# Optimization experiments

Hardware: AMD Instinct MI355X
Metric: run time of the kernel (lower is better)

Reference implementation:

```python
import jax, jax.numpy as jnp
import numpy as np

D, H, DFF, N = 256, 8, 2048, 100
B, T, M1, M2 = 64, 77, 400, 400
DH = D // H
EPS = 1e-5
NEG = -1e9


def _ln(x, w, b):
    m = jnp.mean(x, axis=-1, keepdims=True)
    v = jnp.mean((x - m) ** 2, axis=-1, keepdims=True)
    return (x - m) / jnp.sqrt(v + EPS) * w + b


def _mha(q_in, kv_in, in_w, in_b, out_w, out_b, kpm):
    # q_in: [Tq, D], kv_in: [Tk, D], in_w: [3D, D], kpm: [Tk] bool (True = pad)
    wq, wk, wv = in_w[:D], in_w[D:2 * D], in_w[2 * D:]
    bq, bk, bv = in_b[:D], in_b[D:2 * D], in_b[2 * D:]
    q = (q_in @ wq.T + bq).reshape(-1, H, DH)
    k = (kv_in @ wk.T + bk).reshape(-1, H, DH)
    v = (kv_in @ wv.T + bv).reshape(-1, H, DH)
    scores = jnp.einsum('qhd,khd->hqk', q, k) / np.sqrt(DH).astype(np.float32)
    scores = jnp.where(kpm[None, None, :], NEG, scores)
    attn = jax.nn.softmax(scores, axis=-1)
    out = jnp.einsum('hqk,khd->qhd', attn, v).reshape(-1, D)
    return out @ out_w.T + out_b


def _decoder(x, mem, tmask, mmask, saw, sab, saow, saob,
             caw, cab, caow, caob, l1w, l1b, l2w, l2b,
             n1w, n1b, n2w, n2b, n3w, n3b):
    # Post-norm TransformerDecoderLayer (eval mode, no dropout)
    x = _ln(x + _mha(x, x, saw, sab, saow, saob, tmask), n1w, n1b)
    x = _ln(x + _mha(x, mem, caw, cab, caow, caob, mmask), n2w, n2b)
    ff = jax.nn.relu(x @ l1w.T + l1b) @ l2w.T + l2b
    return _ln(x + ff, n3w, n3b)


def setup_inputs() -> dict:
    key = jax.random.key(0)
    ks = jax.random.split(key, 12)
    s = 0.02
    return {
        'text_embed': jax.random.normal(ks[0], (B, T, D), jnp.float32),
        'text_mask': jnp.zeros((B, T), bool),
        'im_embed1': jax.random.normal(ks[1], (B, M1, D), jnp.float32),
        'im_mask1': jnp.zeros((B, M1), bool),
        'im_embed2': jax.random.normal(ks[2], (B, M2, D), jnp.float32),
        'im_mask2': jnp.zeros((B, M2), bool),
        'sid': jax.random.randint(ks[3], (B,), 0, N),
        'sa_in_w': jax.random.normal(ks[4], (N, 3 * D, D), jnp.float32) * s,
        'sa_in_b': jnp.zeros((N, 3 * D), jnp.float32),
        'sa_out_w': jax.random.normal(ks[5], (N, D, D), jnp.float32) * s,
        'sa_out_b': jnp.zeros((N, D), jnp.float32),
        'ca_in_w': jax.random.normal(ks[6], (N, 3 * D, D), jnp.float32) * s,
        'ca_in_b': jnp.zeros((N, 3 * D), jnp.float32),
        'ca_out_w': jax.random.normal(ks[7], (N, D, D), jnp.float32) * s,
        'ca_out_b': jnp.zeros((N, D), jnp.float32),
        'lin1_w': jax.random.normal(ks[8], (N, DFF, D), jnp.float32) * s,
        'lin1_b': jnp.zeros((N, DFF), jnp.float32),
        'lin2_w': jax.random.normal(ks[9], (N, D, DFF), jnp.float32) * s,
        'lin2_b': jnp.zeros((N, D), jnp.float32),
        'ln1_w': jnp.ones((N, D), jnp.float32),
        'ln1_b': jnp.zeros((N, D), jnp.float32),
        'ln2_w': jnp.ones((N, D), jnp.float32),
        'ln2_b': jnp.zeros((N, D), jnp.float32),
        'ln3_w': jnp.ones((N, D), jnp.float32),
        'ln3_b': jnp.zeros((N, D), jnp.float32),
    }


def reference(text_embed, text_mask, im_embed1, im_mask1, im_embed2, im_mask2, sid,
              sa_in_w, sa_in_b, sa_out_w, sa_out_b,
              ca_in_w, ca_in_b, ca_out_w, ca_out_b,
              lin1_w, lin1_b, lin2_w, lin2_b,
              ln1_w, ln1_b, ln2_w, ln2_b, ln3_w, ln3_b):
    mem = jnp.concatenate([im_embed1, im_embed2], axis=1)    # [B, M1+M2, D]
    mmask = jnp.concatenate([im_mask1, im_mask2], axis=1)    # [B, M1+M2]
    params = tuple(p[sid] for p in (
        sa_in_w, sa_in_b, sa_out_w, sa_out_b,
        ca_in_w, ca_in_b, ca_out_w, ca_out_b,
        lin1_w, lin1_b, lin2_w, lin2_b,
        ln1_w, ln1_b, ln2_w, ln2_b, ln3_w, ln3_b))
    return jax.vmap(_decoder)(text_embed, mem, text_mask, mmask, *params)
```

## Files before the change

### kernel.cpp

```cpp
#include <hip/hip_runtime.h>
#include <hip/hip_bf16.h>
#include <math.h>

constexpr int kB   = 64;
constexpr int kT   = 77;
constexpr int kD   = 256;
constexpr int kH   = 8;
constexpr int kDH  = 32;
constexpr int kDFF = 2048;
constexpr int kM1  = 400;
constexpr int kMKV = 800;
constexpr float kEPS = 1e-5f;
constexpr float kNEG = -1000000000.0f;

typedef __attribute__((ext_vector_type(8))) short short8;
typedef __attribute__((ext_vector_type(4))) float floatx4;
typedef __attribute__((ext_vector_type(16))) float floatx16;

__device__ __forceinline__ unsigned pkbf(float x, float y) {
    unsigned ux = __float_as_uint(x), uy = __float_as_uint(y);
    ux = (ux + 0x7fffu + ((ux >> 16) & 1u)) >> 16;
    uy = (uy + 0x7fffu + ((uy >> 16) & 1u)) & 0xffff0000u;
    return ux | uy;
}
__device__ __forceinline__ unsigned short bf16u(float x) {
    unsigned u = __float_as_uint(x);
    return (unsigned short)((u + 0x7fffu + ((u >> 16) & 1u)) >> 16);
}

__global__ __launch_bounds__(256) void mfma_gemm(
    const float* __restrict__ A1, long long sA1,
    const float* __restrict__ A2, long long sA2, int splitM, int lda,
    const float* __restrict__ W, long long sW, int ldw,
    const float* __restrict__ bias, long long sB,
    float* __restrict__ C, long long sC, int ldc,
    const int* __restrict__ sid, int M, int N, int K, int tilesM, int relu)
{
    __shared__ unsigned short As[128][88];
    __shared__ unsigned short Bs[128][88];

    int b = blockIdx.z;
    int s = sid[b];
    int ty = blockIdx.x % tilesM;
    int tx = blockIdx.x / tilesM;
    int tm0 = ty * 128, tn0 = tx * 128;

    const float* Wb = W + (long long)s * sW;
    const float* Bb = bias + (long long)s * sB;
    float* Cb = C + (long long)b * sC;

    int t = threadIdx.x;
    int lane = t & 63, wv = t >> 6;
    int wm = wv >> 1, wn = wv & 1;
    int q = lane >> 4, mrow = lane & 15;

    floatx4 acc[4][4] = {};

    for (int k0 = 0; k0 < K; k0 += 64) {
        #pragma unroll
        for (int p = 0; p < 8; p++) {
            int row = (t >> 4) + 16 * p;
            int kf  = (t & 15) * 4;
            int ar = tm0 + row;
            float4 v = make_float4(0.f, 0.f, 0.f, 0.f);
            if (ar < M) {
                const float* src = (ar < splitM)
                    ? (A1 + (long long)b * sA1 + (long long)ar * lda)
                    : (A2 + (long long)b * sA2 + (long long)(ar - splitM) * lda);
                v = *(const float4*)(src + k0 + kf);
            }
            *(uint2*)&As[row][kf] = make_uint2(pkbf(v.x, v.y), pkbf(v.z, v.w));
        }
        #pragma unroll
        for (int p = 0; p < 8; p++) {
            int row = (t >> 4) + 16 * p;
            int kf  = (t & 15) * 4;
            const float* src = Wb + (long long)(tn0 + row) * ldw + k0 + kf;
            float4 v = *(const float4*)src;
            *(uint2*)&Bs[row][kf] = make_uint2(pkbf(v.x, v.y), pkbf(v.z, v.w));
        }
        __syncthreads();

        #pragma unroll
        for (int ks = 0; ks < 2; ks++) {
            int kk = ks * 32 + q * 8;
            short8 af[4], bfr[4];
            #pragma unroll
            for (int i = 0; i < 4; i++) {
                af[i]  = *(const short8*)&As[wm * 64 + i * 16 + mrow][kk];
                bfr[i] = *(const short8*)&Bs[wn * 64 + i * 16 + mrow][kk];
            }
            #pragma unroll
            for (int mi = 0; mi < 4; mi++)
                #pragma unroll
                for (int ni = 0; ni < 4; ni++)
                    acc[mi][ni] = __builtin_amdgcn_mfma_f32_16x16x32_bf16(
                        af[mi], bfr[ni], acc[mi][ni], 0, 0, 0);
        }
        __syncthreads();
    }

    #pragma unroll
    for (int ni = 0; ni < 4; ni++) {
        int cgl = tn0 + wn * 64 + ni * 16 + mrow;
        float bv = Bb[cgl];
        #pragma unroll
        for (int mi = 0; mi < 4; mi++) {
            #pragma unroll
            for (int e = 0; e < 4; e++) {
                int r = tm0 + wm * 64 + mi * 16 + q * 4 + e;
                if (r < M) {
                    float o = acc[mi][ni][e] + bv;
                    if (relu) o = fmaxf(o, 0.f);
                    Cb[(long long)r * ldc + cgl] = o;
                }
            }
        }
    }
}

__global__ __launch_bounds__(256) void attn3(
    const float* __restrict__ Q, long long sQ, int ldq,
    const float* __restrict__ Kp, long long sK, int ldk,
    const float* __restrict__ Vp, long long sV, int ldv,
    const unsigned char* __restrict__ m1, int sM1,
    const unsigned char* __restrict__ m2, int sM2,
    int split, int nk, int ntiles,
    float* __restrict__ O, long long sO, int ldo, float scale)
{
    __shared__ __align__(16) char smem[19456];
    unsigned short (*Kl)[40] = (unsigned short (*)[40])(smem);
    unsigned short (*Vt)[36] = (unsigned short (*)[36])(smem + 5120);
    unsigned short (*Ql)[40] = (unsigned short (*)[40])(smem + 7424);
    char* Pbyte = smem + 9984;
    float* mkf  = (float*)(smem + 16128);

    int t = threadIdx.x;
    int qt = blockIdx.x, h = blockIdx.y, b = blockIdx.z;
    int qbase = qt * 32;

    const float* Qb = Q  + (long long)b * sQ + h * kDH;
    const float* Kb = Kp + (long long)b * sK + h * kDH;
    const float* Vb = Vp + (long long)b * sV + h * kDH;

    int lane = t & 63, w = t >> 6;
    int lq = lane & 15, q4 = lane >> 4;
    int d31 = lane & 31, hh = lane >> 5;
    int sj = t >> 2, sd = (t & 3) * 8;

    {
        int q = t >> 3, df = (t & 7) * 4;
        int gq = qbase + q;
        float4 v = make_float4(0.f, 0.f, 0.f, 0.f);
        if (gq < kT) v = *(const float4*)(Qb + (long long)gq * ldq + df);
        *(uint2*)&Ql[q][df] = make_uint2(pkbf(v.x, v.y), pkbf(v.z, v.w));
    }

    float4 ka, kb, va, vb; float mkv = 0.f;
    auto issue_loads = [&](int jt) {
        int gj = jt + sj;
        if (gj < nk) {
            const float* kp = Kb + (long long)gj * ldk + sd;
            const float* vp = Vb + (long long)gj * ldv + sd;
            ka = *(const float4*)kp;  kb = *(const float4*)(kp + 4);
            va = *(const float4*)vp;  vb = *(const float4*)(vp + 4);
        } else {
            ka = kb = va = vb = make_float4(0.f, 0.f, 0.f, 0.f);
        }
        if (t < 64) {
            int tj = jt + t;
            if (tj < nk)
                mkv = ((tj < split) ? m1[b * sM1 + tj] : m2[b * sM2 + (tj - split)])
                        ? kNEG : 0.f;
            else
                mkv = -INFINITY;
        }
    };
    auto write_stage = [&]() {
        *(uint4*)&Kl[sj][sd] = make_uint4(pkbf(ka.x, ka.y), pkbf(ka.z, ka.w),
                                          pkbf(kb.x, kb.y), pkbf(kb.z, kb.w));
        Vt[sd + 0][sj] = bf16u(va.x); Vt[sd + 1][sj] = bf16u(va.y);
        Vt[sd + 2][sj] = bf16u(va.z); Vt[sd + 3][sj] = bf16u(va.w);
        Vt[sd + 4][sj] = bf16u(vb.x); Vt[sd + 5][sj] = bf16u(vb.y);
        Vt[sd + 6][sj] = bf16u(vb.z); Vt[sd + 7][sj] = bf16u(vb.w);
        if (t < 64) mkf[t] = mkv;
    };

    issue_loads(0);
    write_stage();
    __syncthreads();

    short8 Bq0 = *(const short8*)&Ql[lq][8 * q4];
    short8 Bq1 = *(const short8*)&Ql[lq + 16][8 * q4];

    floatx16 accO = {};
    float m0 = -INFINITY, m1v = -INFINITY, l0 = 0.f, l1 = 0.f;
    char* Pw = Pbyte + w * 1536;

    for (int tile = 0; tile < ntiles; tile++) {
        bool pf = (tile + 1 < ntiles);
        if (pf) issue_loads((tile + 1) * 64);

        short8 akf = *(const short8*)&Kl[16 * w + lq][8 * q4];
        floatx4 c0 = {}, c1 = {};
        c0 = __builtin_amdgcn_mfma_f32_16x16x32_bf16(akf, Bq0, c0, 0, 0, 0);
        c1 = __builtin_amdgcn_mfma_f32_16x16x32_bf16(akf, Bq1, c1, 0, 0, 0);

        float mka0 = mkf[16 * w + 4 * q4 + 0];
        float mka1 = mkf[16 * w + 4 * q4 + 1];
        float mka2 = mkf[16 * w + 4 * q4 + 2];
        float mka3 = mkf[16 * w + 4 * q4 + 3];

        float s00 = c0[0] * scale + mka0, s01 = c0[1] * scale + mka1;
        float s02 = c0[2] * scale + mka2, s03 = c0[3] * scale + mka3;
        float s10 = c1[0] * scale + mka0, s11 = c1[1] * scale + mka1;
        float s12 = c1[2] * scale + mka2, s13 = c1[3] * scale + mka3;

        float mt0 = fmaxf(fmaxf(s00, s01), fmaxf(s02, s03));
        float mt1 = fmaxf(fmaxf(s10, s11), fmaxf(s12, s13));
        mt0 = fmaxf(mt0, __shfl_xor(mt0, 16)); mt0 = fmaxf(mt0, __shfl_xor(mt0, 32));
        mt1 = fmaxf(mt1, __shfl_xor(mt1, 16)); mt1 = fmaxf(mt1, __shfl_xor(mt1, 32));
        float mn0 = fmaxf(m0, mt0), mn1 = fmaxf(m1v, mt1);
        float al0 = __expf(m0 - mn0), al1 = __expf(m1v - mn1);

        float p00 = __expf(s00 - mn0), p01 = __expf(s01 - mn0);
        float p02 = __expf(s02 - mn0), p03 = __expf(s03 - mn0);
        float p10 = __expf(s10 - mn1), p11 = __expf(s11 - mn1);
        float p12 = __expf(s12 - mn1), p13 = __expf(s13 - mn1);

        float sum0 = (p00 + p01) + (p02 + p03);
        float sum1 = (p10 + p11) + (p12 + p13);
        sum0 += __shfl_xor(sum0, 16); sum0 += __shfl_xor(sum0, 32);
        sum1 += __shfl_xor(sum1, 16); sum1 += __shfl_xor(sum1, 32);
        l0 = l0 * al0 + sum0;  l1 = l1 * al1 + sum1;
        m0 = mn0;  m1v = mn1;

        *(unsigned*)(Pw + lq * 48 + (8 * q4 + 0))        = pkbf(p00, p01);
        *(unsigned*)(Pw + lq * 48 + (8 * q4 + 4))        = pkbf(p02, p03);
        *(unsigned*)(Pw + (lq + 16) * 48 + ((8 * q4 + 0) ^ 16)) = pkbf(p10, p11);
        *(unsigned*)(Pw + (lq + 16) * 48 + ((8 * q4 + 4) ^ 16)) = pkbf(p12, p13);
        short8 bp = *(const short8*)(Pw + d31 * 48 + ((16 * hh) ^ (d31 & 16)));

        int j0 = 16 * w + 8 * hh;
        uint2 va2 = *(const uint2*)&Vt[d31][j0];
        uint2 vb2 = *(const uint2*)&Vt[d31][j0 + 4];
        union { unsigned u[4]; short8 s; } avu;
        avu.u[0] = va2.x; avu.u[1] = va2.y; avu.u[2] = vb2.x; avu.u[3] = vb2.y;

        float als = (lane & 16) ? al1 : al0;
        #pragma unroll
        for (int e = 0; e < 16; e++) accO[e] *= als;
        accO = __builtin_amdgcn_mfma_f32_32x32x16_bf16(avu.s, bp, accO, 0, 0, 0);

        __syncthreads();
        if (pf) { write_stage(); __syncthreads(); }
    }

    float* Ow = (float*)smem;
    float* ms = (float*)(smem + 18432);
    float* ls = (float*)(smem + 18944);
    #pragma unroll
    for (int g = 0; g < 4; g++) {
        int d0 = 8 * g + 4 * hh;
        float4 ve = make_float4(accO[4 * g + 0], accO[4 * g + 1],
                                accO[4 * g + 2], accO[4 * g + 3]);
        *(float4*)&Ow[(w * 32 + d31) * 36 + d0] = ve;
    }
    if (q4 == 0) {
        ms[w * 32 + lq] = m0;   ms[w * 32 + lq + 16] = m1v;
        ls[w * 32 + lq] = l0;   ls[w * 32 + lq + 16] = l1;
    }
    __syncthreads();
    {
        int qq = t >> 3, db = (t & 7) * 4;
        float mw0 = ms[qq],      mw1 = ms[32 + qq];
        float mw2 = ms[64 + qq], mw3 = ms[96 + qq];
        float M = fmaxf(fmaxf(mw0, mw1), fmaxf(mw2, mw3));
        float e0 = __expf(mw0 - M), e1 = __expf(mw1 - M);
        float e2 = __expf(mw2 - M), e3 = __expf(mw3 - M);
        float L = e0 * ls[qq] + e1 * ls[32 + qq] + e2 * ls[64 + qq] + e3 * ls[96 + qq];
        float inv = 1.f / L;
        float4 o0 = *(const float4*)&Ow[(0 * 32 + qq) * 36 + db];
        float4 o1 = *(const float4*)&Ow[(1 * 32 + qq) * 36 + db];
        float4 o2 = *(const float4*)&Ow[(2 * 32 + qq) * 36 + db];
        float4 o3 = *(const float4*)&Ow[(3 * 32 + qq) * 36 + db];
        float4 o;
        o.x = (e0 * o0.x + e1 * o1.x + e2 * o2.x + e3 * o3.x) * inv;
        o.y = (e0 * o0.y + e1 * o1.y + e2 * o2.y + e3 * o3.y) * inv;
        o.z = (e0 * o0.z + e1 * o1.z + e2 * o2.z + e3 * o3.z) * inv;
        o.w = (e0 * o0.w + e1 * o1.w + e2 * o2.w + e3 * o3.w) * inv;
        int gq = qbase + qq;
        if (gq < kT)
            *(float4*)(O + (long long)b * sO + (long long)gq * ldo + h * kDH + db) = o;
    }
}

__global__ __launch_bounds__(256) void addln_kernel(
    const float* __restrict__ A, const float* __restrict__ R,
    const float* __restrict__ w, const float* __restrict__ bb,
    const int* __restrict__ sid, float* __restrict__ O)
{
    int t = blockIdx.x, b = blockIdx.y, d = threadIdx.x;
    long long base = ((long long)(b * kT + t)) * kD;
    float x = A[base + d] + R[base + d];

    __shared__ float r1[4], r2[4];
    int wid = d >> 6;

    float sacc = x;
    #pragma unroll
    for (int off = 32; off >= 1; off >>= 1) sacc += __shfl_xor(sacc, off);
    if ((d & 63) == 0) r1[wid] = sacc;
    __syncthreads();
    float mean = (r1[0] + r1[1] + r1[2] + r1[3]) * (1.0f / 256.0f);

    float diff = x - mean;
    float s2 = diff * diff;
    #pragma unroll
    for (int off = 32; off >= 1; off >>= 1) s2 += __shfl_xor(s2, off);
    if ((d & 63) == 0) r2[wid] = s2;
    __syncthreads();
    float var = (r2[0] + r2[1] + r2[2] + r2[3]) * (1.0f / 256.0f);

    int s = sid[b];
    float y = diff * rsqrtf(var + kEPS) * w[s * kD + d] + bb[s * kD + d];
    O[base + d] = y;
}

extern "C" void kernel_launch(void* const* d_in, const int* in_sizes, int n_in,
                              void* d_out, int out_size, void* d_ws, size_t ws_size,
                              hipStream_t stream)
{
    const float*         text   = (const float*)d_in[0];
    const unsigned char* tmask  = (const unsigned char*)d_in[1];
    const float*         im1    = (const float*)d_in[2];
    const unsigned char* immk1  = (const unsigned char*)d_in[3];
    const float*         im2    = (const float*)d_in[4];
    const unsigned char* immk2  = (const unsigned char*)d_in[5];
    const int*           sid    = (const int*)d_in[6];
    const float* sa_in_w  = (const float*)d_in[7];
    const float* sa_in_b  = (const float*)d_in[8];
    const float* sa_out_w = (const float*)d_in[9];
    const float* sa_out_b = (const float*)d_in[10];
    const float* ca_in_w  = (const float*)d_in[11];
    const float* ca_in_b  = (const float*)d_in[12];
    const float* ca_out_w = (const float*)d_in[13];
    const float* ca_out_b = (const float*)d_in[14];
    const float* lin1_w   = (const float*)d_in[15];
    const float* lin1_b   = (const float*)d_in[16];
    const float* lin2_w   = (const float*)d_in[17];
    const float* lin2_b   = (const float*)d_in[18];
    const float* ln1_w    = (const float*)d_in[19];
    const float* ln1_b    = (const float*)d_in[20];
    const float* ln2_w    = (const float*)d_in[21];
    const float* ln2_b    = (const float*)d_in[22];
    const float* ln3_w    = (const float*)d_in[23];
    const float* ln3_b    = (const float*)d_in[24];
    float* out = (float*)d_out;

    float* ws = (float*)d_ws;
    float* qkv_sa  = ws;
    float* q_ca    = qkv_sa  + (long long)kB * kT * 768;
    float* kv_ca   = q_ca    + (long long)kB * kT * kD;
    float* attnbuf = kv_ca   + (long long)kB * kMKV * 512;
    float* tmp     = attnbuf + (long long)kB * kT * kD;
    float* x1      = tmp     + (long long)kB * kT * kD;
    float* x2      = x1      + (long long)kB * kT * kD;
    float* hff     = x2      + (long long)kB * kT * kD;

    const float scale = 0.17677669529663687f;
    dim3 blk(256);

    auto gemm = [&](const float* A1, long long sA1, const float* A2, long long sA2,
                    int splitM, int lda,
                    const float* W, long long sW, int ldw,
                    const float* bias, long long sB,
                    float* C, long long sC, int ldc,
                    int M, int N, int K, int relu) {
        int tm = (M + 127) / 128, tn = N / 128;
        mfma_gemm<<<dim3(tm * tn, 1, kB), blk, 0, stream>>>(
            A1, sA1, A2, sA2, splitM, lda, W, sW, ldw, bias, sB,
            C, sC, ldc, sid, M, N, K, tm, relu);
    };

    gemm(text, (long long)kT * kD, text, 0, kT, kD,
         sa_in_w, (long long)3 * kD * kD, kD, sa_in_b, 3 * kD,
         qkv_sa, (long long)kT * 768, 768, kT, 768, kD, 0);

    attn3<<<dim3(3, kH, kB), blk, 0, stream>>>(
        qkv_sa,       (long long)kT * 768, 768,
        qkv_sa + 256, (long long)kT * 768, 768,
        qkv_sa + 512, (long long)kT * 768, 768,
        tmask, kT, tmask, kT, kT, kT, 2,
        attnbuf, (long long)kT * kD, kD, scale);

    gemm(attnbuf, (long long)kT * kD, attnbuf, 0, kT, kD,
         sa_out_w, (long long)kD * kD, kD, sa_out_b, kD,
         tmp, (long long)kT * kD, kD, kT, kD, kD, 0);

    addln_kernel<<<dim3(kT, kB), blk, 0, stream>>>(tmp, text, ln1_w, ln1_b, sid, x1);

    gemm(x1, (long long)kT * kD, x1, 0, kT, kD,
         ca_in_w, (long long)3 * kD * kD, kD, ca_in_b, 3 * kD,
         q_ca, (long long)kT * kD, kD, kT, kD, kD, 0);

    gemm(im1, (long long)kM1 * kD, im2, (long long)kM1 * kD, kM1, kD,
         ca_in_w + (long long)kD * kD, (long long)3 * kD * kD, kD,
         ca_in_b + kD, 3 * kD,
         kv_ca, (long long)kMKV * 512, 512, kMKV, 512, kD, 0);

    attn3<<<dim3(3, kH, kB), blk, 0, stream>>>(
        q_ca,        (long long)kT * kD, kD,
        kv_ca,       (long long)kMKV * 512, 512,
        kv_ca + 256, (long long)kMKV * 512, 512,
        immk1, kM1, immk2, kM1, kM1, kMKV, 13,
        attnbuf, (long long)kT * kD, kD, scale);

    gemm(attnbuf, (long long)kT * kD, attnbuf, 0, kT, kD,
         ca_out_w, (long long)kD * kD, kD, ca_out_b, kD,
         tmp, (long long)kT * kD, kD, kT, kD, kD, 0);

    addln_kernel<<<dim3(kT, kB), blk, 0, stream>>>(tmp, x1, ln2_w, ln2_b, sid, x2);

    gemm(x2, (long long)kT * kD, x2, 0, kT, kD,
         lin1_w, (long long)kDFF * kD, kD, lin1_b, kDFF,
         hff, (long long)kT * kDFF, kDFF, kT, kDFF, kD, 1);

    gemm(hff, (long long)kT * kDFF, hff, 0, kT, kDFF,
         lin2_w, (long long)kD * kDFF, kDFF, lin2_b, kD,
         tmp, (long long)kT * kD, kD, kT, kD, kDFF, 0);

    addln_kernel<<<dim3(kT, kB), blk, 0, stream>>>(tmp, x2, ln3_w, ln3_b, sid, out);
}
```

Measured before the change: 1.006 ms.

## Swizzle GEMM LDS tiles with XOR layout and remap workgroups across XCDs

The padded GEMM shared-memory tiles become dense 128x64 bf16 arrays addressed with an XOR swizzle on the row index, which removes the padding while avoiding LDS bank conflicts. Both GEMM and attention launches switch to a flat 1D grid whose block ids are remapped so that consecutive logical tiles of the same batch item, and therefore the same weight set, land on the same XCD to improve L2 reuse. The remapping adds a few integer divisions per block, and the gain depends on how the hardware dispatches blocks round-robin across XCDs.

```diff
diff --git a/kernel.cpp b/kernel.cpp
--- a/kernel.cpp
+++ b/kernel.cpp
@@ -28,23 +28,31 @@
     return (unsigned short)((u + 0x7fffu + ((u >> 16) & 1u)) >> 16);
 }
 
+__device__ __forceinline__ int xcd_swz(int id, int nwg) {
+    int q = nwg >> 3, r = nwg & 7;
+    int x = id & 7, i = id >> 3;
+    return (x < r ? x * (q + 1) : r * (q + 1) + (x - r) * q) + i;
+}
+
 __global__ __launch_bounds__(256) void mfma_gemm(
     const float* __restrict__ A1, long long sA1,
     const float* __restrict__ A2, long long sA2, int splitM, int lda,
     const float* __restrict__ W, long long sW, int ldw,
     const float* __restrict__ bias, long long sB,
     float* __restrict__ C, long long sC, int ldc,
-    const int* __restrict__ sid, int M, int N, int K, int tilesM, int relu)
+    const int* __restrict__ sid, int M, int N, int K, int tm, int tpb, int relu)
 {
-    __shared__ unsigned short As[128][88];
-    __shared__ unsigned short Bs[128][88];
-
-    int b = blockIdx.z;
+    __shared__ __align__(16) unsigned short As[128 * 64];
+    __shared__ __align__(16) unsigned short Bs[128 * 64];
+
+    int wg = xcd_swz(blockIdx.x, gridDim.x);
+    int b    = wg / tpb;
+    int tile = wg - b * tpb;
+    int tx   = tile / tm;
+    int ty   = tile - tx * tm;
+    int tm0 = ty * 128, tn0 = tx * 128;
+
     int s = sid[b];
-    int ty = blockIdx.x % tilesM;
-    int tx = blockIdx.x / tilesM;
-    int tm0 = ty * 128, tn0 = tx * 128;
-
     const float* Wb = W + (long long)s * sW;
     const float* Bb = bias + (long long)s * sB;
     float* Cb = C + (long long)b * sC;
@@ -53,6 +61,7 @@
     int lane = t & 63, wv = t >> 6;
     int wm = wv >> 1, wn = wv & 1;
     int q = lane >> 4, mrow = lane & 15;
+    int xm = (mrow & 7) << 4;
 
     floatx4 acc[4][4] = {};
 
@@ -69,7 +78,8 @@
                     : (A2 + (long long)b * sA2 + (long long)(ar - splitM) * lda);
                 v = *(const float4*)(src + k0 + kf);
             }
-            *(uint2*)&As[row][kf] = make_uint2(pkbf(v.x, v.y), pkbf(v.z, v.w));
+            int off = ((row << 7) + (kf << 1)) ^ ((row & 7) << 4);
+            *(uint2*)((char*)As + off) = make_uint2(pkbf(v.x, v.y), pkbf(v.z, v.w));
         }
         #pragma unroll
         for (int p = 0; p < 8; p++) {
@@ -77,18 +87,21 @@
             int kf  = (t & 15) * 4;
             const float* src = Wb + (long long)(tn0 + row) * ldw + k0 + kf;
             float4 v = *(const float4*)src;
-            *(uint2*)&Bs[row][kf] = make_uint2(pkbf(v.x, v.y), pkbf(v.z, v.w));
+            int off = ((row << 7) + (kf << 1)) ^ ((row & 7) << 4);
+            *(uint2*)((char*)Bs + off) = make_uint2(pkbf(v.x, v.y), pkbf(v.z, v.w));
         }
         __syncthreads();
 
         #pragma unroll
         for (int ks = 0; ks < 2; ks++) {
-            int kk = ks * 32 + q * 8;
+            int kb = ks * 64 + q * 16;
             short8 af[4], bfr[4];
             #pragma unroll
             for (int i = 0; i < 4; i++) {
-                af[i]  = *(const short8*)&As[wm * 64 + i * 16 + mrow][kk];
-                bfr[i] = *(const short8*)&Bs[wn * 64 + i * 16 + mrow][kk];
+                int ra = wm * 64 + i * 16 + mrow;
+                int rb = wn * 64 + i * 16 + mrow;
+                af[i]  = *(const short8*)((const char*)As + (((ra << 7) + kb) ^ xm));
+                bfr[i] = *(const short8*)((const char*)Bs + (((rb << 7) + kb) ^ xm));
             }
             #pragma unroll
             for (int mi = 0; mi < 4; mi++)
@@ -136,7 +149,11 @@
     float* mkf  = (float*)(smem + 16128);
 
     int t = threadIdx.x;
-    int qt = blockIdx.x, h = blockIdx.y, b = blockIdx.z;
+    int wg = xcd_swz(blockIdx.x, gridDim.x);
+    int b  = wg / 24;
+    int rem = wg - b * 24;
+    int h  = rem / 3;
+    int qt = rem - h * 3;
     int qbase = qt * 32;
 
     const float* Qb = Q  + (long long)b * sQ + h * kDH;
@@ -378,16 +395,17 @@
                     float* C, long long sC, int ldc,
                     int M, int N, int K, int relu) {
         int tm = (M + 127) / 128, tn = N / 128;
-        mfma_gemm<<<dim3(tm * tn, 1, kB), blk, 0, stream>>>(
+        int tpb = tm * tn;
+        mfma_gemm<<<dim3(tpb * kB), blk, 0, stream>>>(
             A1, sA1, A2, sA2, splitM, lda, W, sW, ldw, bias, sB,
-            C, sC, ldc, sid, M, N, K, tm, relu);
+            C, sC, ldc, sid, M, N, K, tm, tpb, relu);
     };
 
     gemm(text, (long long)kT * kD, text, 0, kT, kD,
          sa_in_w, (long long)3 * kD * kD, kD, sa_in_b, 3 * kD,
          qkv_sa, (long long)kT * 768, 768, kT, 768, kD, 0);
 
-    attn3<<<dim3(3, kH, kB), blk, 0, stream>>>(
+    attn3<<<dim3(3 * kH * kB), blk, 0, stream>>>(
         qkv_sa,       (long long)kT * 768, 768,
         qkv_sa + 256, (long long)kT * 768, 768,
         qkv_sa + 512, (long long)kT * 768, 768,
@@ -409,7 +427,7 @@
          ca_in_b + kD, 3 * kD,
          kv_ca, (long long)kMKV * 512, 512, kMKV, 512, kD, 0);
 
-    attn3<<<dim3(3, kH, kB), blk, 0, stream>>>(
+    attn3<<<dim3(3 * kH * kB), blk, 0, stream>>>(
         q_ca,        (long long)kT * kD, kD,
         kv_ca,       (long long)kMKV * 512, 512,
         kv_ca + 256, (long long)kMKV * 512, 512,
```

After: 1.007 ms. No clear change (+0.1%).
